# Performance work log

Measured on AMD Instinct MI355X. Metric: run time of the kernel, lower is better.

Reference implementation:

```python
import jax, jax.numpy as jnp
import numpy as np

N = 50000      # nodes
E = 400000     # edges
IN = 128       # in_dim == emb_dim (residual requires equality)
POS = 64       # pos_in_dim
EMB = 128
LN_EPS = 1e-5


def _ln(x, g, b):
    m = jnp.mean(x, axis=-1, keepdims=True)
    v = jnp.mean((x - m) ** 2, axis=-1, keepdims=True)
    return (x - m) / jnp.sqrt(v + LN_EPS) * g + b


def _gin(x, src, dst, eps, W1, b1, g1, be1, W2, b2):
    # GINConv: mlp((1+eps)*x + sum_{j in N(i)} x_j)
    agg = jax.ops.segment_sum(x[src], dst, num_segments=x.shape[0])
    h = (1.0 + eps) * x + agg
    h = jax.nn.relu(_ln(h @ W1 + b1, g1, be1))
    return h @ W2 + b2


def setup_inputs() -> dict:
    key = jax.random.key(0)
    ks = jax.random.split(key, 8)
    x = jax.random.normal(ks[0], (N, IN), jnp.float32)
    pos = jax.random.normal(ks[1], (N, POS), jnp.float32)
    edge_index = jax.random.randint(ks[2], (2, E), 0, N)
    d = IN + POS
    f32 = jnp.float32
    W1 = (jax.random.normal(ks[3], (d, EMB), f32) / np.sqrt(d))
    W2 = (jax.random.normal(ks[4], (EMB, EMB), f32) / np.sqrt(EMB))
    W1p = (jax.random.normal(ks[5], (POS, EMB), f32) / np.sqrt(POS))
    W2p = (jax.random.normal(ks[6], (EMB, EMB), f32) / np.sqrt(EMB))
    z = jnp.zeros((EMB,), f32)
    o = jnp.ones((EMB,), f32)
    return {
        "x": x, "pos": pos, "edge_index": edge_index,
        "eps": jnp.zeros((), f32), "W1": W1, "b1": z, "g1": o, "be1": z,
        "W2": W2, "b2": z, "ln_g": o, "ln_b": z,
        "epsp": jnp.zeros((), f32), "W1p": W1p, "b1p": z, "g1p": o, "be1p": z,
        "W2p": W2p, "b2p": z, "lnp_g": o, "lnp_b": z,
    }


def reference(x, pos, edge_index, eps, W1, b1, g1, be1, W2, b2, ln_g, ln_b,
              epsp, W1p, b1p, g1p, be1p, W2p, b2p, lnp_g, lnp_b):
    src, dst = edge_index[0], edge_index[1]
    node_feats = jnp.concatenate([x, pos], axis=-1)  # [N, IN+POS]
    h = jax.nn.relu(_ln(_gin(node_feats, src, dst, eps, W1, b1, g1, be1, W2, b2), ln_g, ln_b))
    p = jax.nn.relu(_ln(_gin(pos, src, dst, epsp, W1p, b1p, g1p, be1p, W2p, b2p), lnp_g, lnp_b))
    # dropout is identity in eval mode (model_drop_ratio applied only when training)
    h = h + x  # add_residual=True
    return (h, p)
```

## Files before the change

### kernel.cpp

```cpp
#include <hip/hip_runtime.h>

#define NN    50000
#define NPAD  50048
#define HB    391
#define EE    400000
#define IND   128
#define POSD  64
#define DD    192
#define EMBD  128
#define LNEPS 1e-5f
#define CAP   32

#define PREP_B 4692
#define FILL_B 1563
#define WC_B   256

typedef __attribute__((ext_vector_type(8))) short bf16x8;
typedef __attribute__((ext_vector_type(4))) unsigned short u16x4;
typedef __attribute__((ext_vector_type(4))) float f32x4;
typedef unsigned short ushort_t;
typedef unsigned int uint_t;

#define MFMA16 __builtin_amdgcn_mfma_f32_16x16x32_bf16

__device__ inline ushort_t f2bf(float f) {
  union { float f; unsigned u; } v; v.f = f;
  unsigned r = (v.u + 0x7FFFu + ((v.u >> 16) & 1u)) >> 16;
  return (ushort_t)r;
}
__device__ inline float bf2f(unsigned u) {
  union { unsigned u; float f; } v; v.u = u << 16;
  return v.f;
}

__global__ __launch_bounds__(256) void prep_k(
    const float* __restrict__ x, const float* __restrict__ pos,
    const int* __restrict__ ei,
    const float* __restrict__ W1, const float* __restrict__ W2,
    const float* __restrict__ W1p, const float* __restrict__ W2p,
    int* __restrict__ cnt, int* __restrict__ csr,
    ushort_t* __restrict__ cat, ushort_t* __restrict__ wt) {
  const int bid = blockIdx.x;
  if (bid < PREP_B) {
    int id  = bid * 256 + threadIdx.x;
    int n   = id / 24, sub = id - n * 24;
    bf16x8 o = (bf16x8){0, 0, 0, 0, 0, 0, 0, 0};
    if (n < NN) {
      const float* src = (sub < 16) ? (x + (size_t)n * IND + sub * 8)
                                    : (pos + (size_t)n * POSD + (sub - 16) * 8);
      f32x4 v0 = *(const f32x4*)(src);
      f32x4 v1 = *(const f32x4*)(src + 4);
#pragma unroll
      for (int i = 0; i < 4; ++i) {
        o[i]     = (short)f2bf(v0[i]);
        o[i + 4] = (short)f2bf(v1[i]);
      }
    }
    *(bf16x8*)(cat + (size_t)n * DD + sub * 8) = o;
  } else if (bid < PREP_B + FILL_B) {
    int e = (bid - PREP_B) * 256 + threadIdx.x;
    if (e < EE) {
      int src = ei[e];
      int dst = ei[EE + e];
      int idx = atomicAdd(&cnt[dst], 1);
      if (idx < CAP) csr[(size_t)dst * CAP + idx] = src;
    }
  } else {
    int t = (bid - PREP_B - FILL_B) * 256 + threadIdx.x;
    if (t < 24576) {
      int c = t / 192, k = t % 192;
      wt[t] = f2bf(W1[k * EMBD + c]);
    } else if (t < 40960) {
      int q = t - 24576; int c = q / 128, k = q % 128;
      wt[t] = f2bf(W2[k * EMBD + c]);
    } else if (t < 49152) {
      int q = t - 40960; int c = q / 64, k = q % 64;
      wt[t] = f2bf(W1p[k * EMBD + c]);
    } else {
      int q = t - 49152; int c = q / 128, k = q % 128;
      wt[t] = f2bf(W2p[k * EMBD + c]);
    }
  }
}

__global__ __launch_bounds__(256) void fill_k(
    const int* __restrict__ ei, int* __restrict__ cnt, int* __restrict__ csr) {
  int e = blockIdx.x * 256 + threadIdx.x;
  if (e >= EE) return;
  int src = ei[e];
  int dst = ei[EE + e];
  int idx = atomicAdd(&cnt[dst], 1);
  if (idx < CAP) csr[(size_t)dst * CAP + idx] = src;
}

__global__ __launch_bounds__(256) void wconv_k(
    const float* __restrict__ W1, const float* __restrict__ W2,
    const float* __restrict__ W1p, const float* __restrict__ W2p,
    ushort_t* __restrict__ wt) {
  int tid = blockIdx.x * 256 + threadIdx.x;
  if (tid < 24576) {
    int c = tid / 192, k = tid % 192;
    wt[tid] = f2bf(W1[k * EMBD + c]);
  } else if (tid < 40960) {
    int t = tid - 24576; int c = t / 128, k = t % 128;
    wt[tid] = f2bf(W2[k * EMBD + c]);
  } else if (tid < 49152) {
    int t = tid - 40960; int c = t / 64, k = t % 64;
    wt[tid] = f2bf(W1p[k * EMBD + c]);
  } else {
    int t = tid - 49152; int c = t / 128, k = t % 128;
    wt[tid] = f2bf(W2p[k * EMBD + c]);
  }
}

__global__ __launch_bounds__(256) void gather_k(
    const float* __restrict__ x, const float* __restrict__ pos,
    const int* __restrict__ cnt, const int* __restrict__ csr,
    const float* __restrict__ epsv, const float* __restrict__ epspv,
    ushort_t* __restrict__ h0, ushort_t* __restrict__ p0) {
  const int lane = threadIdx.x & 63;
  const int wv   = threadIdx.x >> 6;
  const int n    = blockIdx.x * 4 + wv;
  if (n >= NPAD) return;

  float a0 = 0.f, a1 = 0.f, a2 = 0.f;
  float xs0 = 0.f, xs1 = 0.f, ps = 0.f;

  if (n < NN) {
    int deg = cnt[n]; if (deg > CAP) deg = CAP;
    const int* row = csr + (size_t)n * CAP;
    int idx = (lane < deg) ? row[lane] : 0;
    int t = 0;
    for (; t + 2 <= deg; t += 2) {
      int s1 = __shfl(idx, t);
      int s2 = __shfl(idx, t + 1);
      a0 += x[(size_t)s1 * IND + lane] + x[(size_t)s2 * IND + lane];
      a1 += x[(size_t)s1 * IND + 64 + lane] + x[(size_t)s2 * IND + 64 + lane];
      a2 += pos[(size_t)s1 * POSD + lane] + pos[(size_t)s2 * POSD + lane];
    }
    if (t < deg) {
      int s1 = __shfl(idx, t);
      a0 += x[(size_t)s1 * IND + lane];
      a1 += x[(size_t)s1 * IND + 64 + lane];
      a2 += pos[(size_t)s1 * POSD + lane];
    }
    xs0 = x[(size_t)n * IND + lane];
    xs1 = x[(size_t)n * IND + 64 + lane];
    ps  = pos[(size_t)n * POSD + lane];
  }

  float e1  = 1.0f + epsv[0];
  float ep1 = 1.0f + epspv[0];
  h0[(size_t)n * DD + lane]       = f2bf(fmaf(e1, xs0, a0));
  h0[(size_t)n * DD + 64 + lane]  = f2bf(fmaf(e1, xs1, a1));
  h0[(size_t)n * DD + 128 + lane] = f2bf(fmaf(e1, ps,  a2));
  p0[(size_t)n * POSD + lane]     = f2bf(fmaf(ep1, ps, a2));
}

__global__ __launch_bounds__(256) void gather2_k(
    const ushort_t* __restrict__ cat, const int* __restrict__ cnt,
    const int* __restrict__ csr,
    const float* __restrict__ epsv, const float* __restrict__ epspv,
    ushort_t* __restrict__ h0, ushort_t* __restrict__ p0) {
  const int lane = threadIdx.x & 63;
  const int wv   = threadIdx.x >> 6;
  const int half = lane >> 5;
  const int l2   = lane & 31;
  const int n    = blockIdx.x * 8 + wv * 2 + half;

  int deg = 0;
  if (n < NN) { deg = cnt[n]; if (deg > CAP) deg = CAP; }
  int idx = (l2 < deg) ? csr[(size_t)n * CAP + l2] : NN;

  float a0 = 0.f, a1 = 0.f, a2 = 0.f, a3 = 0.f, a4 = 0.f, a5 = 0.f;
  for (int t = 0; t < deg; t += 8) {
    int s[8];
#pragma unroll
    for (int k = 0; k < 8; ++k) s[k] = __shfl(idx, half * 32 + t + k);
    u16x4 u[8]; uint_t v[8];
#pragma unroll
    for (int k = 0; k < 8; ++k) {
      int sk = (t + k < CAP) ? s[k] : NN;
      const ushort_t* r = cat + (size_t)sk * DD;
      u[k] = *(const u16x4*)(r + l2 * 4);
      v[k] = *(const uint_t*)(r + 128 + l2 * 2);
    }
#pragma unroll
    for (int k = 0; k < 8; ++k) {
      a0 += bf2f(u[k][0]); a1 += bf2f(u[k][1]);
      a2 += bf2f(u[k][2]); a3 += bf2f(u[k][3]);
      a4 += bf2f(v[k] & 0xffffu); a5 += bf2f(v[k] >> 16);
    }
  }

  const float e1  = 1.0f + epsv[0];
  const float ep1 = 1.0f + epspv[0];
  const ushort_t* self = cat + (size_t)n * DD;
  u16x4 su = *(const u16x4*)(self + l2 * 4);
  uint_t sv = *(const uint_t*)(self + 128 + l2 * 2);

  u16x4 o;
  o[0] = f2bf(fmaf(e1, bf2f(su[0]), a0));
  o[1] = f2bf(fmaf(e1, bf2f(su[1]), a1));
  o[2] = f2bf(fmaf(e1, bf2f(su[2]), a2));
  o[3] = f2bf(fmaf(e1, bf2f(su[3]), a3));
  *(u16x4*)(h0 + (size_t)n * DD + l2 * 4) = o;

  float p4 = bf2f(sv & 0xffffu), p5 = bf2f(sv >> 16);
  uint_t oh = (uint_t)f2bf(fmaf(e1, p4, a4)) |
              ((uint_t)f2bf(fmaf(e1, p5, a5)) << 16);
  *(uint_t*)(h0 + (size_t)n * DD + 128 + l2 * 2) = oh;
  uint_t op = (uint_t)f2bf(fmaf(ep1, p4, a4)) |
              ((uint_t)f2bf(fmaf(ep1, p5, a5)) << 16);
  *(uint_t*)(p0 + (size_t)n * POSD + l2 * 2) = op;
}

__device__ inline void ln_epi_T(f32x4 (&acc)[8][2],
                                const float* __restrict__ bias,
                                const float* __restrict__ gam,
                                const float* __restrict__ bet, int g) {
  f32x4 bv[8], gv[8], bev[8];
#pragma unroll
  for (int nt = 0; nt < 8; ++nt) {
    bv[nt]  = *(const f32x4*)(bias + nt * 16 + g * 4);
    gv[nt]  = *(const f32x4*)(gam  + nt * 16 + g * 4);
    bev[nt] = *(const f32x4*)(bet  + nt * 16 + g * 4);
  }
#pragma unroll
  for (int mt = 0; mt < 2; ++mt) {
    float s = 0.f, sq = 0.f;
#pragma unroll
    for (int nt = 0; nt < 8; ++nt)
#pragma unroll
      for (int r = 0; r < 4; ++r) {
        float v = acc[nt][mt][r] + bv[nt][r];
        acc[nt][mt][r] = v;
        s += v; sq += v * v;
      }
    s  += __shfl_xor(s, 16);  sq += __shfl_xor(sq, 16);
    s  += __shfl_xor(s, 32);  sq += __shfl_xor(sq, 32);
    float mean = s * (1.0f / 128.0f);
    float var  = sq * (1.0f / 128.0f) - mean * mean;
    float rstd = rsqrtf(var + LNEPS);
#pragma unroll
    for (int nt = 0; nt < 8; ++nt)
#pragma unroll
      for (int r = 0; r < 4; ++r)
        acc[nt][mt][r] = fmaxf(
            fmaf((acc[nt][mt][r] - mean) * rstd, gv[nt][r], bev[nt][r]), 0.f);
  }
}

__device__ inline void act_write_T(char* act, f32x4 (&acc)[8][2], int g, int c0) {
#pragma unroll
  for (int mt = 0; mt < 2; ++mt) {
    int lr = mt * 16 + c0;
    int sw = (lr & 7) << 4;
#pragma unroll
    for (int nt = 0; nt < 8; ++nt) {
      u16x4 o;
#pragma unroll
      for (int r = 0; r < 4; ++r) o[r] = f2bf(acc[nt][mt][r]);
      *(u16x4*)(act + lr * 256 + ((nt * 32 + g * 8) ^ sw)) = o;
    }
  }
}

__device__ inline void stage_w(const ushort_t* __restrict__ src, char* dst,
                               int rowbytes, int chunks, int tid) {
  int cpr = rowbytes >> 4;
  for (int i = tid; i < chunks; i += 256) {
    int row  = i / cpr;
    int colb = (i - row * cpr) << 4;
    *(bf16x8*)(dst + row * rowbytes + (colb ^ ((row & 7) << 4))) =
        *(const bf16x8*)(src + (size_t)i * 8);
  }
}

__global__ __launch_bounds__(256) void mlp_k(
    const ushort_t* __restrict__ h0, const ushort_t* __restrict__ p0,
    const ushort_t* __restrict__ wt,
    const float* __restrict__ b1, const float* __restrict__ g1,
    const float* __restrict__ be1,
    const float* __restrict__ b2, const float* __restrict__ lng,
    const float* __restrict__ lnb,
    const float* __restrict__ b1p, const float* __restrict__ g1p,
    const float* __restrict__ be1p,
    const float* __restrict__ b2p, const float* __restrict__ lnpg,
    const float* __restrict__ lnpb,
    const float* __restrict__ x, float* __restrict__ out) {
  __shared__ __align__(16) char smem[81920];
  const int tid  = threadIdx.x;
  const int lane = tid & 63;
  const int wv   = tid >> 6;
  const int g    = lane >> 4;
  const int c0   = lane & 15;
  const int bid  = blockIdx.x;
  char* act = smem + 49152 + wv * 8192;

  f32x4 acc[8][2];

  if (bid < HB) {
    const int m0 = bid * 128;
    stage_w(wt, smem, 384, 3072, tid);
    bf16x8 a0[6], a1[6];
    const size_t r0 = (size_t)(m0 + wv * 32 + c0) * DD;
    const size_t r1 = r0 + (size_t)16 * DD;
#pragma unroll
    for (int ks = 0; ks < 6; ++ks) {
      a0[ks] = *(const bf16x8*)(h0 + r0 + ks * 32 + g * 8);
      a1[ks] = *(const bf16x8*)(h0 + r1 + ks * 32 + g * 8);
    }
    __syncthreads();

#pragma unroll
    for (int nt = 0; nt < 8; ++nt)
#pragma unroll
      for (int mt = 0; mt < 2; ++mt) acc[nt][mt] = (f32x4){0.f, 0.f, 0.f, 0.f};
#pragma unroll
    for (int ks = 0; ks < 6; ++ks)
#pragma unroll
      for (int nt = 0; nt < 8; ++nt) {
        int wrow = nt * 16 + c0;
        bf16x8 w = *(const bf16x8*)(smem + wrow * 384 +
                                    ((ks * 64 + g * 16) ^ ((wrow & 7) << 4)));
        acc[nt][0] = MFMA16(w, a0[ks], acc[nt][0], 0, 0, 0);
        acc[nt][1] = MFMA16(w, a1[ks], acc[nt][1], 0, 0, 0);
      }
    ln_epi_T(acc, b1, g1, be1, g);
    act_write_T(act, acc, g, c0);
    __syncthreads();
    stage_w(wt + 24576, smem, 256, 2048, tid);
    __syncthreads();

#pragma unroll
    for (int nt = 0; nt < 8; ++nt)
#pragma unroll
      for (int mt = 0; mt < 2; ++mt) acc[nt][mt] = (f32x4){0.f, 0.f, 0.f, 0.f};
#pragma unroll
    for (int ks = 0; ks < 4; ++ks) {
      bf16x8 am[2];
#pragma unroll
      for (int mt = 0; mt < 2; ++mt) {
        int lr = mt * 16 + c0;
        am[mt] = *(const bf16x8*)(act + lr * 256 +
                                  ((ks * 64 + g * 16) ^ ((lr & 7) << 4)));
      }
#pragma unroll
      for (int nt = 0; nt < 8; ++nt) {
        int wrow = nt * 16 + c0;
        bf16x8 w = *(const bf16x8*)(smem + wrow * 256 +
                                    ((ks * 64 + g * 16) ^ ((wrow & 7) << 4)));
        acc[nt][0] = MFMA16(w, am[0], acc[nt][0], 0, 0, 0);
        acc[nt][1] = MFMA16(w, am[1], acc[nt][1], 0, 0, 0);
      }
    }
    ln_epi_T(acc, b2, lng, lnb, g);
#pragma unroll
    for (int mt = 0; mt < 2; ++mt) {
      int node = m0 + wv * 32 + mt * 16 + c0;
      if (node < NN) {
#pragma unroll
        for (int nt = 0; nt < 8; ++nt) {
          int f0 = nt * 16 + g * 4;
          f32x4 xr = *(const f32x4*)(x + (size_t)node * IND + f0);
          f32x4 o;
#pragma unroll
          for (int r = 0; r < 4; ++r) o[r] = acc[nt][mt][r] + xr[r];
          *(f32x4*)(out + (size_t)node * EMBD + f0) = o;
        }
      }
    }
  } else {
    const int m0 = (bid - HB) * 128;
    stage_w(wt + 40960, smem, 128, 1024, tid);
    stage_w(wt + 49152, smem + 16384, 256, 2048, tid);
    bf16x8 a0[2], a1[2];
    const size_t r0 = (size_t)(m0 + wv * 32 + c0) * POSD;
    const size_t r1 = r0 + (size_t)16 * POSD;
#pragma unroll
    for (int ks = 0; ks < 2; ++ks) {
      a0[ks] = *(const bf16x8*)(p0 + r0 + ks * 32 + g * 8);
      a1[ks] = *(const bf16x8*)(p0 + r1 + ks * 32 + g * 8);
    }
    __syncthreads();

#pragma unroll
    for (int nt = 0; nt < 8; ++nt)
#pragma unroll
      for (int mt = 0; mt < 2; ++mt) acc[nt][mt] = (f32x4){0.f, 0.f, 0.f, 0.f};
#pragma unroll
    for (int ks = 0; ks < 2; ++ks)
#pragma unroll
      for (int nt = 0; nt < 8; ++nt) {
        int wrow = nt * 16 + c0;
        bf16x8 w = *(const bf16x8*)(smem + wrow * 128 +
                                    ((ks * 64 + g * 16) ^ ((wrow & 7) << 4)));
        acc[nt][0] = MFMA16(w, a0[ks], acc[nt][0], 0, 0, 0);
        acc[nt][1] = MFMA16(w, a1[ks], acc[nt][1], 0, 0, 0);
      }
    ln_epi_T(acc, b1p, g1p, be1p, g);
    act_write_T(act, acc, g, c0);

#pragma unroll
    for (int nt = 0; nt < 8; ++nt)
#pragma unroll
      for (int mt = 0; mt < 2; ++mt) acc[nt][mt] = (f32x4){0.f, 0.f, 0.f, 0.f};
#pragma unroll
    for (int ks = 0; ks < 4; ++ks) {
      bf16x8 am[2];
#pragma unroll
      for (int mt = 0; mt < 2; ++mt) {
        int lr = mt * 16 + c0;
        am[mt] = *(const bf16x8*)(act + lr * 256 +
                                  ((ks * 64 + g * 16) ^ ((lr & 7) << 4)));
      }
#pragma unroll
      for (int nt = 0; nt < 8; ++nt) {
        int wrow = nt * 16 + c0;
        bf16x8 w = *(const bf16x8*)(smem + 16384 + wrow * 256 +
                                    ((ks * 64 + g * 16) ^ ((wrow & 7) << 4)));
        acc[nt][0] = MFMA16(w, am[0], acc[nt][0], 0, 0, 0);
        acc[nt][1] = MFMA16(w, am[1], acc[nt][1], 0, 0, 0);
      }
    }
    ln_epi_T(acc, b2p, lnpg, lnpb, g);
#pragma unroll
    for (int mt = 0; mt < 2; ++mt) {
      int node = m0 + wv * 32 + mt * 16 + c0;
      if (node < NN) {
#pragma unroll
        for (int nt = 0; nt < 8; ++nt) {
          int f0 = nt * 16 + g * 4;
          f32x4 o;
#pragma unroll
          for (int r = 0; r < 4; ++r) o[r] = acc[nt][mt][r];
          *(f32x4*)(out + (size_t)NN * EMBD + (size_t)node * EMBD + f0) = o;
        }
      }
    }
  }
}

extern "C" void kernel_launch(void* const* d_in, const int* in_sizes, int n_in,
                              void* d_out, int out_size, void* d_ws, size_t ws_size,
                              hipStream_t stream) {
  const float* x    = (const float*)d_in[0];
  const float* pos  = (const float*)d_in[1];
  const int*   ei   = (const int*)d_in[2];
  const float* eps  = (const float*)d_in[3];
  const float* W1   = (const float*)d_in[4];
  const float* b1   = (const float*)d_in[5];
  const float* g1   = (const float*)d_in[6];
  const float* be1  = (const float*)d_in[7];
  const float* W2   = (const float*)d_in[8];
  const float* b2   = (const float*)d_in[9];
  const float* lng  = (const float*)d_in[10];
  const float* lnb  = (const float*)d_in[11];
  const float* epsp = (const float*)d_in[12];
  const float* W1p  = (const float*)d_in[13];
  const float* b1p  = (const float*)d_in[14];
  const float* g1p  = (const float*)d_in[15];
  const float* be1p = (const float*)d_in[16];
  const float* W2p  = (const float*)d_in[17];
  const float* b2p  = (const float*)d_in[18];
  const float* lnpg = (const float*)d_in[19];
  const float* lnpb = (const float*)d_in[20];

  char* ws = (char*)d_ws;
  float* out = (float*)d_out;

  const size_t CATB = (size_t)NPAD * DD * 2;
  const size_t P0B  = (size_t)NPAD * POSD * 2;
  const size_t NEED_BIG = 200000 + 6400000 + CATB + CATB + P0B + 131072;

  int* cnt = (int*)ws;
  int* csr = (int*)(ws + 200000);

  hipMemsetAsync(cnt, 0, (size_t)NN * sizeof(int), stream);

  if (ws_size >= NEED_BIG) {
    ushort_t* cat = (ushort_t*)(ws + 6600000);
    ushort_t* h0  = (ushort_t*)(ws + 6600000 + CATB);
    ushort_t* p0  = (ushort_t*)(ws + 6600000 + 2 * CATB);
    ushort_t* wt  = (ushort_t*)(ws + 6600000 + 2 * CATB + P0B);

    prep_k<<<PREP_B + FILL_B + WC_B, 256, 0, stream>>>(
        x, pos, ei, W1, W2, W1p, W2p, cnt, csr, cat, wt);
    gather2_k<<<NPAD / 8, 256, 0, stream>>>(cat, cnt, csr, eps, epsp, h0, p0);
    mlp_k<<<2 * HB, 256, 0, stream>>>(
        h0, p0, wt, b1, g1, be1, b2, lng, lnb,
        b1p, g1p, be1p, b2p, lnpg, lnpb, x, out);
  } else {
    ushort_t* h0 = (ushort_t*)(ws + 6600000);
    ushort_t* p0 = (ushort_t*)(ws + 6600000 + CATB);
    ushort_t* wt = (ushort_t*)(ws + 6600000 + CATB + P0B);

    fill_k<<<(EE + 255) / 256, 256, 0, stream>>>(ei, cnt, csr);
    wconv_k<<<256, 256, 0, stream>>>(W1, W2, W1p, W2p, wt);
    gather_k<<<NPAD / 4, 256, 0, stream>>>(x, pos, cnt, csr, eps, epsp, h0, p0);
    mlp_k<<<2 * HB, 256, 0, stream>>>(
        h0, p0, wt, b1, g1, be1, b2, lng, lnb,
        b1p, g1p, be1p, b2p, lnpg, lnpb, x, out);
  }
}
```

Before: 113.6 us.

## Split fused MLP kernel into two passes with bf16 intermediate in global memory

The single MLP kernel, which ran both linear layers per tile with 80KB of shared memory, is split into two kernels. The first computes linear1, LayerNorm and ReLU and writes a tiled bf16 intermediate (h1/p1) to workspace. The second stages W2 and finishes linear2, LayerNorm and the residual. This lowers shared memory per block and drops the mid-kernel barriers and weight restaging, aiming for higher occupancy, at the cost of an extra launch and a global round trip of the intermediate. The small-workspace fallback path is removed, and h1/p1 overlap the cnt/csr region, which is assumed dead by then.

```diff
diff --git a/kernel.cpp b/kernel.cpp
--- a/kernel.cpp
+++ b/kernel.cpp
@@ -83,80 +83,6 @@
   }
 }
 
-__global__ __launch_bounds__(256) void fill_k(
-    const int* __restrict__ ei, int* __restrict__ cnt, int* __restrict__ csr) {
-  int e = blockIdx.x * 256 + threadIdx.x;
-  if (e >= EE) return;
-  int src = ei[e];
-  int dst = ei[EE + e];
-  int idx = atomicAdd(&cnt[dst], 1);
-  if (idx < CAP) csr[(size_t)dst * CAP + idx] = src;
-}
-
-__global__ __launch_bounds__(256) void wconv_k(
-    const float* __restrict__ W1, const float* __restrict__ W2,
-    const float* __restrict__ W1p, const float* __restrict__ W2p,
-    ushort_t* __restrict__ wt) {
-  int tid = blockIdx.x * 256 + threadIdx.x;
-  if (tid < 24576) {
-    int c = tid / 192, k = tid % 192;
-    wt[tid] = f2bf(W1[k * EMBD + c]);
-  } else if (tid < 40960) {
-    int t = tid - 24576; int c = t / 128, k = t % 128;
-    wt[tid] = f2bf(W2[k * EMBD + c]);
-  } else if (tid < 49152) {
-    int t = tid - 40960; int c = t / 64, k = t % 64;
-    wt[tid] = f2bf(W1p[k * EMBD + c]);
-  } else {
-    int t = tid - 49152; int c = t / 128, k = t % 128;
-    wt[tid] = f2bf(W2p[k * EMBD + c]);
-  }
-}
-
-__global__ __launch_bounds__(256) void gather_k(
-    const float* __restrict__ x, const float* __restrict__ pos,
-    const int* __restrict__ cnt, const int* __restrict__ csr,
-    const float* __restrict__ epsv, const float* __restrict__ epspv,
-    ushort_t* __restrict__ h0, ushort_t* __restrict__ p0) {
-  const int lane = threadIdx.x & 63;
-  const int wv   = threadIdx.x >> 6;
-  const int n    = blockIdx.x * 4 + wv;
-  if (n >= NPAD) return;
-
-  float a0 = 0.f, a1 = 0.f, a2 = 0.f;
-  float xs0 = 0.f, xs1 = 0.f, ps = 0.f;
-
-  if (n < NN) {
-    int deg = cnt[n]; if (deg > CAP) deg = CAP;
-    const int* row = csr + (size_t)n * CAP;
-    int idx = (lane < deg) ? row[lane] : 0;
-    int t = 0;
-    for (; t + 2 <= deg; t += 2) {
-      int s1 = __shfl(idx, t);
-      int s2 = __shfl(idx, t + 1);
-      a0 += x[(size_t)s1 * IND + lane] + x[(size_t)s2 * IND + lane];
-      a1 += x[(size_t)s1 * IND + 64 + lane] + x[(size_t)s2 * IND + 64 + lane];
-      a2 += pos[(size_t)s1 * POSD + lane] + pos[(size_t)s2 * POSD + lane];
-    }
-    if (t < deg) {
-      int s1 = __shfl(idx, t);
-      a0 += x[(size_t)s1 * IND + lane];
-      a1 += x[(size_t)s1 * IND + 64 + lane];
-      a2 += pos[(size_t)s1 * POSD + lane];
-    }
-    xs0 = x[(size_t)n * IND + lane];
-    xs1 = x[(size_t)n * IND + 64 + lane];
-    ps  = pos[(size_t)n * POSD + lane];
-  }
-
-  float e1  = 1.0f + epsv[0];
-  float ep1 = 1.0f + epspv[0];
-  h0[(size_t)n * DD + lane]       = f2bf(fmaf(e1, xs0, a0));
-  h0[(size_t)n * DD + 64 + lane]  = f2bf(fmaf(e1, xs1, a1));
-  h0[(size_t)n * DD + 128 + lane] = f2bf(fmaf(e1, ps,  a2));
-  p0[(size_t)n * POSD + lane]     = f2bf(fmaf(ep1, ps, a2));
-}
-
 __global__ __launch_bounds__(256) void gather2_k(
     const ushort_t* __restrict__ cat, const int* __restrict__ cnt,
     const int* __restrict__ csr,
@@ -251,21 +177,6 @@
   }
 }
 
-__device__ inline void act_write_T(char* act, f32x4 (&acc)[8][2], int g, int c0) {
-#pragma unroll
-  for (int mt = 0; mt < 2; ++mt) {
-    int lr = mt * 16 + c0;
-    int sw = (lr & 7) << 4;
-#pragma unroll
-    for (int nt = 0; nt < 8; ++nt) {
-      u16x4 o;
-#pragma unroll
-      for (int r = 0; r < 4; ++r) o[r] = f2bf(acc[nt][mt][r]);
-      *(u16x4*)(act + lr * 256 + ((nt * 32 + g * 8) ^ sw)) = o;
-    }
-  }
-}
-
 __device__ inline void stage_w(const ushort_t* __restrict__ src, char* dst,
                                int rowbytes, int chunks, int tid) {
   int cpr = rowbytes >> 4;
@@ -277,26 +188,21 @@
   }
 }
 
-__global__ __launch_bounds__(256) void mlp_k(
+__global__ __launch_bounds__(256) void mlpA_k(
     const ushort_t* __restrict__ h0, const ushort_t* __restrict__ p0,
     const ushort_t* __restrict__ wt,
     const float* __restrict__ b1, const float* __restrict__ g1,
     const float* __restrict__ be1,
-    const float* __restrict__ b2, const float* __restrict__ lng,
-    const float* __restrict__ lnb,
     const float* __restrict__ b1p, const float* __restrict__ g1p,
     const float* __restrict__ be1p,
-    const float* __restrict__ b2p, const float* __restrict__ lnpg,
-    const float* __restrict__ lnpb,
-    const float* __restrict__ x, float* __restrict__ out) {
-  __shared__ __align__(16) char smem[81920];
+    ushort_t* __restrict__ h1, ushort_t* __restrict__ p1) {
+  __shared__ __align__(16) char smem[49152];
   const int tid  = threadIdx.x;
   const int lane = tid & 63;
   const int wv   = tid >> 6;
   const int g    = lane >> 4;
   const int c0   = lane & 15;
   const int bid  = blockIdx.x;
-  char* act = smem + 49152 + wv * 8192;
 
   f32x4 acc[8][2];
 
@@ -328,53 +234,20 @@
         acc[nt][1] = MFMA16(w, a1[ks], acc[nt][1], 0, 0, 0);
       }
     ln_epi_T(acc, b1, g1, be1, g);
-    act_write_T(act, acc, g, c0);
-    __syncthreads();
-    stage_w(wt + 24576, smem, 256, 2048, tid);
-    __syncthreads();
-
-#pragma unroll
-    for (int nt = 0; nt < 8; ++nt)
-#pragma unroll
-      for (int mt = 0; mt < 2; ++mt) acc[nt][mt] = (f32x4){0.f, 0.f, 0.f, 0.f};
-#pragma unroll
-    for (int ks = 0; ks < 4; ++ks) {
-      bf16x8 am[2];
-#pragma unroll
-      for (int mt = 0; mt < 2; ++mt) {
-        int lr = mt * 16 + c0;
-        am[mt] = *(const bf16x8*)(act + lr * 256 +
-                                  ((ks * 64 + g * 16) ^ ((lr & 7) << 4)));
-      }
+#pragma unroll
+    for (int mt = 0; mt < 2; ++mt) {
+      size_t tb = (size_t)((m0 >> 4) + wv * 2 + mt) * 2048;
 #pragma unroll
       for (int nt = 0; nt < 8; ++nt) {
-        int wrow = nt * 16 + c0;
-        bf16x8 w = *(const bf16x8*)(smem + wrow * 256 +
-                                    ((ks * 64 + g * 16) ^ ((wrow & 7) << 4)));
-        acc[nt][0] = MFMA16(w, am[0], acc[nt][0], 0, 0, 0);
-        acc[nt][1] = MFMA16(w, am[1], acc[nt][1], 0, 0, 0);
-      }
-    }
-    ln_epi_T(acc, b2, lng, lnb, g);
-#pragma unroll
-    for (int mt = 0; mt < 2; ++mt) {
-      int node = m0 + wv * 32 + mt * 16 + c0;
-      if (node < NN) {
-#pragma unroll
-        for (int nt = 0; nt < 8; ++nt) {
-          int f0 = nt * 16 + g * 4;
-          f32x4 xr = *(const f32x4*)(x + (size_t)node * IND + f0);
-          f32x4 o;
-#pragma unroll
-          for (int r = 0; r < 4; ++r) o[r] = acc[nt][mt][r] + xr[r];
-          *(f32x4*)(out + (size_t)node * EMBD + f0) = o;
-        }
+        u16x4 o;
+#pragma unroll
+        for (int r = 0; r < 4; ++r) o[r] = f2bf(acc[nt][mt][r]);
+        *(u16x4*)(h1 + tb + ((nt * 4 + g) * 16 + c0) * 4) = o;
       }
     }
   } else {
     const int m0 = (bid - HB) * 128;
     stage_w(wt + 40960, smem, 128, 1024, tid);
-    stage_w(wt + 49152, smem + 16384, 256, 2048, tid);
     bf16x8 a0[2], a1[2];
     const size_t r0 = (size_t)(m0 + wv * 32 + c0) * POSD;
     const size_t r1 = r0 + (size_t)16 * POSD;
@@ -400,30 +273,88 @@
         acc[nt][1] = MFMA16(w, a1[ks], acc[nt][1], 0, 0, 0);
       }
     ln_epi_T(acc, b1p, g1p, be1p, g);
-    act_write_T(act, acc, g, c0);
-
-#pragma unroll
-    for (int nt = 0; nt < 8; ++nt)
-#pragma unroll
-      for (int mt = 0; mt < 2; ++mt) acc[nt][mt] = (f32x4){0.f, 0.f, 0.f, 0.f};
-#pragma unroll
-    for (int ks = 0; ks < 4; ++ks) {
-      bf16x8 am[2];
-#pragma unroll
-      for (int mt = 0; mt < 2; ++mt) {
-        int lr = mt * 16 + c0;
-        am[mt] = *(const bf16x8*)(act + lr * 256 +
-                                  ((ks * 64 + g * 16) ^ ((lr & 7) << 4)));
-      }
+#pragma unroll
+    for (int mt = 0; mt < 2; ++mt) {
+      size_t tb = (size_t)((m0 >> 4) + wv * 2 + mt) * 2048;
 #pragma unroll
       for (int nt = 0; nt < 8; ++nt) {
-        int wrow = nt * 16 + c0;
-        bf16x8 w = *(const bf16x8*)(smem + 16384 + wrow * 256 +
-                                    ((ks * 64 + g * 16) ^ ((wrow & 7) << 4)));
-        acc[nt][0] = MFMA16(w, am[0], acc[nt][0], 0, 0, 0);
-        acc[nt][1] = MFMA16(w, am[1], acc[nt][1], 0, 0, 0);
-      }
-    }
+        u16x4 o;
+#pragma unroll
+        for (int r = 0; r < 4; ++r) o[r] = f2bf(acc[nt][mt][r]);
+        *(u16x4*)(p1 + tb + ((nt * 4 + g) * 16 + c0) * 4) = o;
+      }
+    }
+  }
+}
+
+__global__ __launch_bounds__(256) void mlpB_k(
+    const ushort_t* __restrict__ h1, const ushort_t* __restrict__ p1,
+    const ushort_t* __restrict__ wt,
+    const float* __restrict__ b2, const float* __restrict__ lng,
+    const float* __restrict__ lnb,
+    const float* __restrict__ b2p, const float* __restrict__ lnpg,
+    const float* __restrict__ lnpb,
+    const float* __restrict__ x, float* __restrict__ out) {
+  __shared__ __align__(16) char smem[32768];
+  const int tid  = threadIdx.x;
+  const int lane = tid & 63;
+  const int wv   = tid >> 6;
+  const int g    = lane >> 4;
+  const int c0   = lane & 15;
+  const int bid  = blockIdx.x;
+  const bool hbr = (bid < HB);
+  const int m0   = (hbr ? bid : bid - HB) * 128;
+  const ushort_t* a_src = hbr ? h1 : p1;
+
+  stage_w(hbr ? (wt + 24576) : (wt + 49152), smem, 256, 2048, tid);
+
+  bf16x8 am[4][2];
+#pragma unroll
+  for (int ks = 0; ks < 4; ++ks)
+#pragma unroll
+    for (int mt = 0; mt < 2; ++mt) {
+      size_t tb = (size_t)((m0 >> 4) + wv * 2 + mt) * 2048;
+      union { u16x4 q[2]; bf16x8 v; } u;
+      u.q[0] = *(const u16x4*)(a_src + tb + ((ks * 8 + g * 2) * 16 + c0) * 4);
+      u.q[1] = *(const u16x4*)(a_src + tb + ((ks * 8 + g * 2 + 1) * 16 + c0) * 4);
+      am[ks][mt] = u.v;
+    }
+  __syncthreads();
+
+  f32x4 acc[8][2];
+#pragma unroll
+  for (int nt = 0; nt < 8; ++nt)
+#pragma unroll
+    for (int mt = 0; mt < 2; ++mt) acc[nt][mt] = (f32x4){0.f, 0.f, 0.f, 0.f};
+#pragma unroll
+  for (int ks = 0; ks < 4; ++ks)
+#pragma unroll
+    for (int nt = 0; nt < 8; ++nt) {
+      int wrow = nt * 16 + c0;
+      bf16x8 w = *(const bf16x8*)(smem + wrow * 256 +
+                                  ((ks * 64 + g * 16) ^ ((wrow & 7) << 4)));
+      acc[nt][0] = MFMA16(w, am[ks][0], acc[nt][0], 0, 0, 0);
+      acc[nt][1] = MFMA16(w, am[ks][1], acc[nt][1], 0, 0, 0);
+    }
+
+  if (hbr) {
+    ln_epi_T(acc, b2, lng, lnb, g);
+#pragma unroll
+    for (int mt = 0; mt < 2; ++mt) {
+      int node = m0 + wv * 32 + mt * 16 + c0;
+      if (node < NN) {
+#pragma unroll
+        for (int nt = 0; nt < 8; ++nt) {
+          int f0 = nt * 16 + g * 4;
+          f32x4 xr = *(const f32x4*)(x + (size_t)node * IND + f0);
+          f32x4 o;
+#pragma unroll
+          for (int r = 0; r < 4; ++r) o[r] = acc[nt][mt][r] + xr[r];
+          *(f32x4*)(out + (size_t)node * EMBD + f0) = o;
+        }
+      }
+    }
+  } else {
     ln_epi_T(acc, b2p, lnpg, lnpb, g);
 #pragma unroll
     for (int mt = 0; mt < 2; ++mt) {
@@ -471,36 +402,24 @@
   float* out = (float*)d_out;
 
   const size_t CATB = (size_t)NPAD * DD * 2;
-  const size_t P0B  = (size_t)NPAD * POSD * 2;
-  const size_t NEED_BIG = 200000 + 6400000 + CATB + CATB + P0B + 131072;
-
-  int* cnt = (int*)ws;
-  int* csr = (int*)(ws + 200000);
+  const size_t H1B  = (size_t)NPAD * EMBD * 2;
+
+  int*      cnt = (int*)ws;
+  int*      csr = (int*)(ws + 200000);
+  ushort_t* cat = (ushort_t*)(ws + 6600000);
+  ushort_t* h0  = (ushort_t*)(ws + 6600000 + CATB);
+  ushort_t* p0  = (ushort_t*)(ws + 6600000 + 2 * CATB);
+  ushort_t* wt  = (ushort_t*)(ws + 6600000 + 2 * CATB +
+                              (size_t)NPAD * POSD * 2);
+  ushort_t* h1  = (ushort_t*)ws;
+  ushort_t* p1  = (ushort_t*)(ws + H1B);
 
   hipMemsetAsync(cnt, 0, (size_t)NN * sizeof(int), stream);
-
-  if (ws_size >= NEED_BIG) {
-    ushort_t* cat = (ushort_t*)(ws + 6600000);
-    ushort_t* h0  = (ushort_t*)(ws + 6600000 + CATB);
-    ushort_t* p0  = (ushort_t*)(ws + 6600000 + 2 * CATB);
-    ushort_t* wt  = (ushort_t*)(ws + 6600000 + 2 * CATB + P0B);
-
-    prep_k<<<PREP_B + FILL_B + WC_B, 256, 0, stream>>>(
-        x, pos, ei, W1, W2, W1p, W2p, cnt, csr, cat, wt);
-    gather2_k<<<NPAD / 8, 256, 0, stream>>>(cat, cnt, csr, eps, epsp, h0, p0);
-    mlp_k<<<2 * HB, 256, 0, stream>>>(
-        h0, p0, wt, b1, g1, be1, b2, lng, lnb,
-        b1p, g1p, be1p, b2p, lnpg, lnpb, x, out);
-  } else {
-    ushort_t* h0 = (ushort_t*)(ws + 6600000);
-    ushort_t* p0 = (ushort_t*)(ws + 6600000 + CATB);
-    ushort_t* wt = (ushort_t*)(ws + 6600000 + CATB + P0B);
-
-    fill_k<<<(EE + 255) / 256, 256, 0, stream>>>(ei, cnt, csr);
-    wconv_k<<<256, 256, 0, stream>>>(W1, W2, W1p, W2p, wt);
-    gather_k<<<NPAD / 4, 256, 0, stream>>>(x, pos, cnt, csr, eps, epsp, h0, p0);
-    mlp_k<<<2 * HB, 256, 0, stream>>>(
-        h0, p0, wt, b1, g1, be1, b2, lng, lnb,
-        b1p, g1p, be1p, b2p, lnpg, lnpb, x, out);
-  }
-}
+  prep_k<<<PREP_B + FILL_B + WC_B, 256, 0, stream>>>(
+      x, pos, ei, W1, W2, W1p, W2p, cnt, csr, cat, wt);
+  gather2_k<<<NPAD / 8, 256, 0, stream>>>(cat, cnt, csr, eps, epsp, h0, p0);
+  mlpA_k<<<2 * HB, 256, 0, stream>>>(
+      h0, p0, wt, b1, g1, be1, b1p, g1p, be1p, h1, p1);
+  mlpB_k<<<2 * HB, 256, 0, stream>>>(
+      h1, p1, wt, b2, lng, lnb, b2p, lnpg, lnpb, x, out);
+}
```

After: 117.7 us. 3.7% more time.
